# Performance work log

Measured on AMD Instinct MI355X. Metric: run time of the kernel, lower is better.

The kernel has to match this reference:

```python
import jax, jax.numpy as jnp
import numpy as np

N_NODES = 50000
N_EDGES = 800000
IN_DIM = 64
OUT_DIM = 64
HID = OUT_DIM // 2  # 32
N_LAYERS = 9  # layer_num; layer_num >= 7 => no temporal conv, conv dropout unused


def _layernorm(x, w, b, eps=1e-5):
    mu = jnp.mean(x, axis=-1, keepdims=True)
    var = jnp.var(x, axis=-1, keepdims=True)
    return (x - mu) * jax.lax.rsqrt(var + eps) * w + b


def _conv(x, Wp, Wn, Ws, src, tgt, pos_m, neg_m):
    # relation-wise gather -> linear -> masked merge -> single scatter_add
    xs = x[src]  # [E, d_in]
    m = jnp.where(pos_m[:, None], xs @ Wp.T, 0.0) + jnp.where(neg_m[:, None], xs @ Wn.T, 0.0)
    agg = jax.ops.segment_sum(m, tgt, num_segments=N_NODES)
    return agg + x @ Ws.T


def _asfr(x, ln_w, ln_b, gw, gb):
    xn = _layernorm(x, ln_w, ln_b)
    w = jax.nn.sigmoid(xn @ gw.T + gb)
    w1 = jnp.where(w > 0.5, 1.0, w)
    w2 = jnp.where(w > 0.5, 0.0, w)
    x1 = w1 * x
    x2 = w2 * x
    h = x.shape[1] // 2
    return jnp.concatenate([x1[:, :h] + x2[:, h:], x1[:, h:] + x2[:, :h]], axis=1)


def setup_inputs() -> dict:
    key = jax.random.key(0)
    ks = jax.random.split(key, 24)
    init_emb = jax.random.normal(ks[0], (N_NODES, IN_DIM), dtype=jnp.float32)
    src = jax.random.randint(ks[1], (N_EDGES,), 0, N_NODES)
    tgt = jax.random.randint(ks[2], (N_EDGES,), 0, N_NODES)
    sign = jnp.where(jax.random.uniform(ks[3], (N_EDGES,)) > 0.5, 1, -1).astype(jnp.int64)
    edge_index_s = jnp.stack([src, tgt, sign], axis=1).astype(jnp.int64)

    def w(k, shape, fan_in):
        return jax.random.normal(k, shape, dtype=jnp.float32) * (1.0 / np.sqrt(fan_in))

    inp = dict(init_emb=init_emb, edge_index_s=edge_index_s)
    # conv1: in 64 -> 32, relations pos/neg + self loop (no bias)
    inp["W1_pos"] = w(ks[4], (HID, IN_DIM), IN_DIM)
    inp["W1_neg"] = w(ks[5], (HID, IN_DIM), IN_DIM)
    inp["W1_self"] = w(ks[6], (HID, IN_DIM), IN_DIM)
    # 8 further convs: 32 -> 32, stacked
    L = N_LAYERS - 1
    inp["Wl_pos"] = w(ks[7], (L, HID, HID), HID)
    inp["Wl_neg"] = w(ks[8], (L, HID, HID), HID)
    inp["Wl_self"] = w(ks[9], (L, HID, HID), HID)
    # ASFR
    inp["asfr_ln_w"] = jnp.ones((HID,), jnp.float32)
    inp["asfr_ln_b"] = jnp.zeros((HID,), jnp.float32)
    inp["asfr_gate_w"] = w(ks[10], (HID, HID), HID)
    inp["asfr_gate_b"] = jnp.zeros((HID,), jnp.float32)
    # projection 32 -> 64
    inp["proj_w"] = w(ks[11], (OUT_DIM, HID), HID)
    inp["proj_b"] = jnp.zeros((OUT_DIM,), jnp.float32)
    # readout MLP: 64 -> 64 -> 64 -> 1, layernorm + relu between
    inp["mlp_w1"] = w(ks[12], (OUT_DIM, OUT_DIM), OUT_DIM)
    inp["mlp_b1"] = jnp.zeros((OUT_DIM,), jnp.float32)
    inp["mlp_ln1_w"] = jnp.ones((OUT_DIM,), jnp.float32)
    inp["mlp_ln1_b"] = jnp.zeros((OUT_DIM,), jnp.float32)
    inp["mlp_w2"] = w(ks[13], (OUT_DIM, OUT_DIM), OUT_DIM)
    inp["mlp_b2"] = jnp.zeros((OUT_DIM,), jnp.float32)
    inp["mlp_ln2_w"] = jnp.ones((OUT_DIM,), jnp.float32)
    inp["mlp_ln2_b"] = jnp.zeros((OUT_DIM,), jnp.float32)
    inp["mlp_w3"] = w(ks[14], (1, OUT_DIM), OUT_DIM)
    inp["mlp_b3"] = jnp.zeros((1,), jnp.float32)
    return inp


def reference(init_emb, edge_index_s, W1_pos, W1_neg, W1_self, Wl_pos, Wl_neg, Wl_self,
              asfr_ln_w, asfr_ln_b, asfr_gate_w, asfr_gate_b, proj_w, proj_b,
              mlp_w1, mlp_b1, mlp_ln1_w, mlp_ln1_b, mlp_w2, mlp_b2,
              mlp_ln2_w, mlp_ln2_b, mlp_w3, mlp_b3):
    src = edge_index_s[:, 0]
    tgt = edge_index_s[:, 1]
    sign = edge_index_s[:, 2]
    pos_m = sign > 0
    neg_m = sign < 0

    z = jax.nn.elu(_conv(init_emb, W1_pos, W1_neg, W1_self, src, tgt, pos_m, neg_m))
    z = _asfr(z, asfr_ln_w, asfr_ln_b, asfr_gate_w, asfr_gate_b)
    for i in range(Wl_pos.shape[0]):
        z_new = jax.nn.elu(_conv(z, Wl_pos[i], Wl_neg[i], Wl_self[i], src, tgt, pos_m, neg_m))
        z = z_new if i == 0 else z_new + 0.1 * z
    z = jax.nn.elu(z @ proj_w.T + proj_b)
    # readout MLP (eval mode: dropout identity)
    h = jax.nn.relu(_layernorm(z @ mlp_w1.T + mlp_b1, mlp_ln1_w, mlp_ln1_b))
    h = jax.nn.relu(_layernorm(h @ mlp_w2.T + mlp_b2, mlp_ln2_w, mlp_ln2_b))
    prob = jax.nn.sigmoid(h @ mlp_w3.T + mlp_b3)
    return (z, prob)
```

## Files before the change

### kernel.cpp

```cpp
#include <hip/hip_runtime.h>
#include <hip/hip_bf16.h>

#define NODES 50000
#define EDGES 800000
#define BSH 8
#define NBUCK 196
#define NBIN_BLOCKS 391

__device__ __forceinline__ float elu1(float x) { return x > 0.f ? x : expm1f(x); }

union F4 { float4 v; float f[4]; };

__global__ __launch_bounds__(256) void k_bhist(const int* __restrict__ ei, int* __restrict__ bucket_cnt) {
  __shared__ int cnt[NBUCK];
  int t = threadIdx.x;
  for (int i = t; i < NBUCK; i += 256) cnt[i] = 0;
  __syncthreads();
  int base = blockIdx.x * 2048;
#pragma unroll
  for (int i = 0; i < 8; i++) {
    int e = base + i * 256 + t;
    if (e < EDGES) atomicAdd(&cnt[ei[e * 3 + 1] >> BSH], 1);
  }
  __syncthreads();
  for (int i = t; i < NBUCK; i += 256)
    if (cnt[i]) atomicAdd(bucket_cnt + i, cnt[i]);
}

__global__ __launch_bounds__(256) void k_bscan(const int* __restrict__ bucket_cnt,
                                               int* __restrict__ bucket_base,
                                               int* __restrict__ bucket_cursor) {
  __shared__ int s[256];
  int t = threadIdx.x;
  int v = (t < NBUCK) ? bucket_cnt[t] : 0;
  s[t] = v;
  __syncthreads();
  for (int o = 1; o < 256; o <<= 1) {
    int x = (t >= o) ? s[t - o] : 0;
    __syncthreads();
    s[t] += x;
    __syncthreads();
  }
  if (t < NBUCK) { int e = s[t] - v; bucket_base[t] = e; bucket_cursor[t] = e; }
}

__global__ __launch_bounds__(256) void k_bin(const int* __restrict__ ei,
                                             int* __restrict__ bucket_cursor,
                                             unsigned* __restrict__ binned) {
  __shared__ int cnt[NBUCK], basec[NBUCK];
  int t = threadIdx.x;
  for (int i = t; i < NBUCK; i += 256) cnt[i] = 0;
  __syncthreads();
  int eb = blockIdx.x * 2048;
#pragma unroll
  for (int i = 0; i < 8; i++) {
    int e = eb + i * 256 + t;
    if (e < EDGES) atomicAdd(&cnt[ei[e * 3 + 1] >> BSH], 1);
  }
  __syncthreads();
  for (int i = t; i < NBUCK; i += 256) {
    int c = cnt[i];
    basec[i] = c ? atomicAdd(bucket_cursor + i, c) : 0;
    cnt[i] = 0;
  }
  __syncthreads();
#pragma unroll
  for (int i = 0; i < 8; i++) {
    int e = eb + i * 256 + t;
    if (e < EDGES) {
      int src = ei[e * 3 + 0];
      int tgt = ei[e * 3 + 1];
      int sg  = ei[e * 3 + 2];
      unsigned val = (unsigned)src | (sg < 0 ? 0x10000u : 0u) | ((unsigned)(tgt & 255) << 17);
      int bkt = tgt >> BSH;
      int r = atomicAdd(&cnt[bkt], 1);
      binned[basec[bkt] + r] = val;
    }
  }
}

__global__ __launch_bounds__(256) void k_scatter2(const unsigned* __restrict__ binned,
                                                  const int* __restrict__ bucket_base,
                                                  const int* __restrict__ bucket_cnt,
                                                  int* __restrict__ offs,
                                                  unsigned* __restrict__ perm) {
  __shared__ int cnt[256];
  __shared__ int s[256];
  int b = blockIdx.x, t = threadIdx.x;
  int t0 = b << BSH;
  cnt[t] = 0;
  __syncthreads();
  int n = bucket_cnt[b], bb = bucket_base[b];
  for (int i = t; i < n; i += 256) atomicAdd(&cnt[(binned[bb + i] >> 17) & 255], 1);
  __syncthreads();
  int v = cnt[t];
  s[t] = v;
  __syncthreads();
  for (int o = 1; o < 256; o <<= 1) {
    int x = (t >= o) ? s[t - o] : 0;
    __syncthreads();
    s[t] += x;
    __syncthreads();
  }
  int pos = bb + s[t] - v;
  if (t0 + t < NODES) offs[t0 + t] = pos;
  cnt[t] = pos;
  if (b == 0 && t == 0) offs[NODES] = EDGES;
  __syncthreads();
  for (int i = t; i < n; i += 256) {
    unsigned e = binned[bb + i];
    int p = atomicAdd(&cnt[(e >> 17) & 255], 1);
    perm[p] = (e & 0xFFFFu) | ((e & 0x10000u) << 15);
  }
}

__global__ __launch_bounds__(256) void k_lin64(const float* __restrict__ x,
    const float* __restrict__ Wp, const float* __restrict__ Wn, const float* __restrict__ Ws,
    __hip_bfloat16* __restrict__ ypb, __hip_bfloat16* __restrict__ ynb,
    unsigned short* __restrict__ ysb) {
  constexpr int K4 = 16;
  __shared__ float4 wp[K4][32], wn[K4][32], wsm[K4][32];
  __shared__ float4 xs[8][K4];
  for (int i = threadIdx.x; i < 32 * K4; i += 256) {
    int k4 = i >> 5, c = i & 31;
    wp[k4][c]  = ((const float4*)Wp)[c * K4 + k4];
    wn[k4][c]  = ((const float4*)Wn)[c * K4 + k4];
    wsm[k4][c] = ((const float4*)Ws)[c * K4 + k4];
  }
  int base = blockIdx.x * 8;
  for (int i = threadIdx.x; i < 8 * K4; i += 256) {
    int r = i / K4, k4 = i - r * K4;
    xs[r][k4] = ((const float4*)(x + (size_t)(base + r) * 64))[k4];
  }
  __syncthreads();
  int lane = threadIdx.x & 31, local = threadIdx.x >> 5;
  float ap = 0.f, an = 0.f, asf = 0.f;
#pragma unroll
  for (int k4 = 0; k4 < K4; k4++) {
    float4 xv = xs[local][k4];
    float4 a = wp[k4][lane], b = wn[k4][lane], c = wsm[k4][lane];
    ap  = fmaf(xv.w, a.w, fmaf(xv.z, a.z, fmaf(xv.y, a.y, fmaf(xv.x, a.x, ap))));
    an  = fmaf(xv.w, b.w, fmaf(xv.z, b.z, fmaf(xv.y, b.y, fmaf(xv.x, b.x, an))));
    asf = fmaf(xv.w, c.w, fmaf(xv.z, c.z, fmaf(xv.y, c.y, fmaf(xv.x, c.x, asf))));
  }
  size_t o = (size_t)(base + local) * 32 + lane;
  ypb[o] = __float2bfloat16(ap);
  ynb[o] = __float2bfloat16(an);
  ysb[o] = __bfloat16_as_ushort(__float2bfloat16(asf));
}

#define ACC8(A, V)                                   \
  A[0] += __uint_as_float((V).x << 16);              \
  A[1] += __uint_as_float((V).x & 0xffff0000u);      \
  A[2] += __uint_as_float((V).y << 16);              \
  A[3] += __uint_as_float((V).y & 0xffff0000u);      \
  A[4] += __uint_as_float((V).z << 16);              \
  A[5] += __uint_as_float((V).z & 0xffff0000u);      \
  A[6] += __uint_as_float((V).w << 16);              \
  A[7] += __uint_as_float((V).w & 0xffff0000u);

template <int DO_ASFR, int DO_RES, int DO_LIN, int WRITE_Z>
__global__ __launch_bounds__(256) void k_layer(
    const unsigned short* __restrict__ ypi, const unsigned short* __restrict__ yni,
    unsigned short* __restrict__ ysb,
    const unsigned* __restrict__ perm, const int* __restrict__ offs,
    float* __restrict__ z,
    const float* __restrict__ lnw, const float* __restrict__ lnb,
    const float* __restrict__ gw, const float* __restrict__ gb,
    const float* __restrict__ Wp, const float* __restrict__ Wn, const float* __restrict__ Ws,
    __hip_bfloat16* __restrict__ ypo, __hip_bfloat16* __restrict__ yno) {
  __shared__ float4 wps[8][32], wns[8][32], wss[8][32], gws[8][32];
  __shared__ float zrow[8][36], xrow[8][36];
  int t = threadIdx.x;
  if (DO_LIN) {
    int k4 = t >> 5, c = t & 31;
    wps[k4][c] = ((const float4*)Wp)[c * 8 + k4];
    wns[k4][c] = ((const float4*)Wn)[c * 8 + k4];
    wss[k4][c] = ((const float4*)Ws)[c * 8 + k4];
    if (DO_ASFR) gws[k4][c] = ((const float4*)gw)[c * 8 + k4];
  }
  int lane = t & 31, local = t >> 5;
  int node = blockIdx.x * 8 + local;
  int es = lane >> 2, fs = lane & 3;
  int beg = offs[node], end = offs[node + 1];
  float a0[8], a1[8], a2[8], a3[8];
#pragma unroll
  for (int i = 0; i < 8; i++) { a0[i] = 0.f; a1[i] = 0.f; a2[i] = 0.f; a3[i] = 0.f; }
  for (int base = beg; base < end; base += 32) {
    unsigned pe = (base + lane < end) ? perm[base + lane] : 0u;
    int rem = end - base;
    unsigned u0 = __shfl(pe, es, 32);
    unsigned u1 = __shfl(pe, es + 8, 32);
    const unsigned short* p0 = (u0 >> 31) ? yni : ypi;
    const unsigned short* p1 = (u1 >> 31) ? yni : ypi;
    uint4 v0 = *((const uint4*)(p0 + (size_t)(u0 & 0x7FFFFFFFu) * 32) + fs);
    uint4 v1 = *((const uint4*)(p1 + (size_t)(u1 & 0x7FFFFFFFu) * 32) + fs);
    if (es < rem) { ACC8(a0, v0); }
    if (es + 8 < rem) { ACC8(a1, v1); }
    if (rem > 16) {
      unsigned u2 = __shfl(pe, es + 16, 32);
      unsigned u3 = __shfl(pe, es + 24, 32);
      const unsigned short* p2 = (u2 >> 31) ? yni : ypi;
      const unsigned short* p3 = (u3 >> 31) ? yni : ypi;
      uint4 v2 = *((const uint4*)(p2 + (size_t)(u2 & 0x7FFFFFFFu) * 32) + fs);
      uint4 v3 = *((const uint4*)(p3 + (size_t)(u3 & 0x7FFFFFFFu) * 32) + fs);
      if (es + 16 < rem) { ACC8(a2, v2); }
      if (es + 24 < rem) { ACC8(a3, v3); }
    }
  }
#pragma unroll
  for (int i = 0; i < 8; i++) a0[i] += (a1[i] + a2[i]) + a3[i];
#pragma unroll
  for (int m = 4; m <= 16; m <<= 1) {
#pragma unroll
    for (int i = 0; i < 8; i++) a0[i] += __shfl_xor(a0[i], m, 32);
  }
  if (es == 0) {
    uint4 sv = *((const uint4*)(ysb + (size_t)node * 32) + fs);
    float sf[8];
    sf[0] = __uint_as_float(sv.x << 16); sf[1] = __uint_as_float(sv.x & 0xffff0000u);
    sf[2] = __uint_as_float(sv.y << 16); sf[3] = __uint_as_float(sv.y & 0xffff0000u);
    sf[4] = __uint_as_float(sv.z << 16); sf[5] = __uint_as_float(sv.z & 0xffff0000u);
    sf[6] = __uint_as_float(sv.w << 16); sf[7] = __uint_as_float(sv.w & 0xffff0000u);
    float o[8];
#pragma unroll
    for (int i = 0; i < 8; i++) o[i] = elu1(a0[i] + sf[i]);
    if (DO_RES) {
      const float* rr = z + (size_t)node * 32 + fs * 8;
      F4 r0, r1;
      r0.v = *(const float4*)rr;
      r1.v = *(const float4*)(rr + 4);
#pragma unroll
      for (int i = 0; i < 4; i++) { o[i] += 0.1f * r0.f[i]; o[4 + i] += 0.1f * r1.f[i]; }
    }
#pragma unroll
    for (int i = 0; i < 8; i++) zrow[local][fs * 8 + i] = o[i];
    if (WRITE_Z) {
      float* zw = z + (size_t)node * 32 + fs * 8;
      *(float4*)zw = make_float4(o[0], o[1], o[2], o[3]);
      *(float4*)(zw + 4) = make_float4(o[4], o[5], o[6], o[7]);
    }
  }
  __syncthreads();
  if (!DO_LIN) return;
  if (DO_ASFR) {
    float v = zrow[local][lane];
    float s = v;
#pragma unroll
    for (int m = 16; m; m >>= 1) s += __shfl_xor(s, m, 32);
    float mu = s * (1.f / 32.f);
    float d = v - mu, sq = d * d;
#pragma unroll
    for (int m = 16; m; m >>= 1) sq += __shfl_xor(sq, m, 32);
    float xn = d * rsqrtf(sq * (1.f / 32.f) + 1e-5f) * lnw[lane] + lnb[lane];
    xrow[local][lane] = xn;
    float ga = gb[lane];
#pragma unroll
    for (int k4 = 0; k4 < 8; k4++) {
      float4 xv = *((const float4*)&xrow[local][0] + k4);
      float4 w = gws[k4][lane];
      ga = fmaf(xv.w, w.w, fmaf(xv.z, w.z, fmaf(xv.y, w.y, fmaf(xv.x, w.x, ga))));
    }
    float g = 1.f / (1.f + __expf(-ga));
    float w1 = g > 0.5f ? 1.f : g;
    float w2 = g > 0.5f ? 0.f : g;
    float zn = w1 * v + __shfl_xor(w2 * v, 16, 32);
    zrow[local][lane] = zn;
  }
  float ap = 0.f, an = 0.f, asf = 0.f;
#pragma unroll
  for (int k4 = 0; k4 < 8; k4++) {
    float4 xv = *((const float4*)&zrow[local][0] + k4);
    float4 a2w = wps[k4][lane], b2 = wns[k4][lane], c2 = wss[k4][lane];
    ap  = fmaf(xv.w, a2w.w, fmaf(xv.z, a2w.z, fmaf(xv.y, a2w.y, fmaf(xv.x, a2w.x, ap))));
    an  = fmaf(xv.w, b2.w, fmaf(xv.z, b2.z, fmaf(xv.y, b2.y, fmaf(xv.x, b2.x, an))));
    asf = fmaf(xv.w, c2.w, fmaf(xv.z, c2.z, fmaf(xv.y, c2.y, fmaf(xv.x, c2.x, asf))));
  }
  size_t o = (size_t)node * 32 + lane;
  ypo[o] = __float2bfloat16(ap);
  yno[o] = __float2bfloat16(an);
  ysb[o] = __bfloat16_as_ushort(__float2bfloat16(asf));
}

__global__ __launch_bounds__(256) void k_mlp(const float* __restrict__ z,
    const float* __restrict__ pw, const float* __restrict__ pb,
    const float* __restrict__ w1, const float* __restrict__ b1,
    const float* __restrict__ l1w, const float* __restrict__ l1b,
    const float* __restrict__ w2, const float* __restrict__ b2,
    const float* __restrict__ l2w, const float* __restrict__ l2b,
    const float* __restrict__ w3, const float* __restrict__ b3,
    float* __restrict__ outz, float* __restrict__ outp) {
  __shared__ float4 wbuf[1536];
  __shared__ float4 hbuf4[128 * 17];
  __shared__ float pb_s[64], b1_s[64], l1w_s[64], l1b_s[64], b2_s[64], l2w_s[64], l2b_s[64], w3_s[64];
  int t = threadIdx.x;
  for (int i = t; i < 512; i += 256) {
    int k = i >> 4, j4 = i & 15;
    float4 v;
    v.x = pw[(j4 * 4 + 0) * 32 + k]; v.y = pw[(j4 * 4 + 1) * 32 + k];
    v.z = pw[(j4 * 4 + 2) * 32 + k]; v.w = pw[(j4 * 4 + 3) * 32 + k];
    wbuf[i] = v;
  }
  for (int i = t; i < 1024; i += 256) {
    int k = i >> 4, j4 = i & 15;
    float4 v;
    v.x = w1[(j4 * 4 + 0) * 64 + k]; v.y = w1[(j4 * 4 + 1) * 64 + k];
    v.z = w1[(j4 * 4 + 2) * 64 + k]; v.w = w1[(j4 * 4 + 3) * 64 + k];
    wbuf[512 + i] = v;
  }
  if (t < 64) {
    pb_s[t] = pb[t]; b1_s[t] = b1[t]; l1w_s[t] = l1w[t]; l1b_s[t] = l1b[t];
    b2_s[t] = b2[t]; l2w_s[t] = l2w[t]; l2b_s[t] = l2b[t]; w3_s[t] = w3[t];
  }
  __syncthreads();
  int g = t >> 3, q = t & 7;
  int nb0 = blockIdx.x * 128 + g;
  float bb3 = b3[0];
  bool live[4];
#pragma unroll
  for (int n = 0; n < 4; n++) live[n] = (nb0 + 32 * n) < NODES;
  float acc[4][8], h[4][8];
#pragma unroll
  for (int n = 0; n < 4; n++)
    if (live[n])
      hbuf4[(n * 32 + g) * 17 + q] = ((const float4*)(z + (size_t)(nb0 + 32 * n) * 32))[q];
#pragma unroll
  for (int n = 0; n < 4; n++)
#pragma unroll
    for (int i = 0; i < 8; i++) acc[n][i] = pb_s[q * 8 + i];
#pragma unroll 2
  for (int k4 = 0; k4 < 8; k4++) {
    F4 hv[4];
#pragma unroll
    for (int n = 0; n < 4; n++) hv[n].v = hbuf4[(n * 32 + g) * 17 + k4];
#pragma unroll
    for (int c = 0; c < 4; c++) {
      float4 wa = wbuf[(k4 * 4 + c) * 16 + q * 2];
      float4 wb = wbuf[(k4 * 4 + c) * 16 + q * 2 + 1];
#pragma unroll
      for (int n = 0; n < 4; n++) {
        float hk = hv[n].f[c];
        acc[n][0] = fmaf(hk, wa.x, acc[n][0]); acc[n][1] = fmaf(hk, wa.y, acc[n][1]);
        acc[n][2] = fmaf(hk, wa.z, acc[n][2]); acc[n][3] = fmaf(hk, wa.w, acc[n][3]);
        acc[n][4] = fmaf(hk, wb.x, acc[n][4]); acc[n][5] = fmaf(hk, wb.y, acc[n][5]);
        acc[n][6] = fmaf(hk, wb.z, acc[n][6]); acc[n][7] = fmaf(hk, wb.w, acc[n][7]);
      }
    }
  }
#pragma unroll
  for (int n = 0; n < 4; n++) {
#pragma unroll
    for (int i = 0; i < 8; i++) h[n][i] = elu1(acc[n][i]);
    float4 h0 = make_float4(h[n][0], h[n][1], h[n][2], h[n][3]);
    float4 h1 = make_float4(h[n][4], h[n][5], h[n][6], h[n][7]);
    if (live[n]) {
      float4* oz = (float4*)(outz + (size_t)(nb0 + 32 * n) * 64 + q * 8);
      oz[0] = h0; oz[1] = h1;
    }
    hbuf4[(n * 32 + g) * 17 + 2 * q] = h0;
    hbuf4[(n * 32 + g) * 17 + 2 * q + 1] = h1;
  }
#pragma unroll
  for (int n = 0; n < 4; n++)
#pragma unroll
    for (int i = 0; i < 8; i++) acc[n][i] = b1_s[q * 8 + i];
#pragma unroll 2
  for (int k4 = 0; k4 < 16; k4++) {
    F4 hv[4];
#pragma unroll
    for (int n = 0; n < 4; n++) hv[n].v = hbuf4[(n * 32 + g) * 17 + k4];
#pragma unroll
    for (int c = 0; c < 4; c++) {
      float4 wa = wbuf[512 + (k4 * 4 + c) * 16 + q * 2];
      float4 wb = wbuf[512 + (k4 * 4 + c) * 16 + q * 2 + 1];
#pragma unroll
      for (int n = 0; n < 4; n++) {
        float hk = hv[n].f[c];
        acc[n][0] = fmaf(hk, wa.x, acc[n][0]); acc[n][1] = fmaf(hk, wa.y, acc[n][1]);
        acc[n][2] = fmaf(hk, wa.z, acc[n][2]); acc[n][3] = fmaf(hk, wa.w, acc[n][3]);
        acc[n][4] = fmaf(hk, wb.x, acc[n][4]); acc[n][5] = fmaf(hk, wb.y, acc[n][5]);
        acc[n][6] = fmaf(hk, wb.z, acc[n][6]); acc[n][7] = fmaf(hk, wb.w, acc[n][7]);
      }
    }
  }
  __syncthreads();
  for (int i = t; i < 1024; i += 256) {
    int k = i >> 4, j4 = i & 15;
    float4 v;
    v.x = w2[(j4 * 4 + 0) * 64 + k]; v.y = w2[(j4 * 4 + 1) * 64 + k];
    v.z = w2[(j4 * 4 + 2) * 64 + k]; v.w = w2[(j4 * 4 + 3) * 64 + k];
    wbuf[i] = v;
  }
#pragma unroll
  for (int n = 0; n < 4; n++) {
    float s = 0.f;
#pragma unroll
    for (int i = 0; i < 8; i++) s += acc[n][i];
    s += __shfl_xor(s, 1, 8); s += __shfl_xor(s, 2, 8); s += __shfl_xor(s, 4, 8);
    float mu = s * (1.f / 64.f);
    float vs = 0.f;
#pragma unroll
    for (int i = 0; i < 8; i++) { float dd = acc[n][i] - mu; vs += dd * dd; }
    vs += __shfl_xor(vs, 1, 8); vs += __shfl_xor(vs, 2, 8); vs += __shfl_xor(vs, 4, 8);
    float rs = rsqrtf(vs * (1.f / 64.f) + 1e-5f);
#pragma unroll
    for (int i = 0; i < 8; i++)
      h[n][i] = fmaxf((acc[n][i] - mu) * rs * l1w_s[q * 8 + i] + l1b_s[q * 8 + i], 0.f);
  }
  __syncthreads();
#pragma unroll
  for (int n = 0; n < 4; n++) {
    hbuf4[(n * 32 + g) * 17 + 2 * q] = make_float4(h[n][0], h[n][1], h[n][2], h[n][3]);
    hbuf4[(n * 32 + g) * 17 + 2 * q + 1] = make_float4(h[n][4], h[n][5], h[n][6], h[n][7]);
  }
#pragma unroll
  for (int n = 0; n < 4; n++)
#pragma unroll
    for (int i = 0; i < 8; i++) acc[n][i] = b2_s[q * 8 + i];
#pragma unroll 2
  for (int k4 = 0; k4 < 16; k4++) {
    F4 hv[4];
#pragma unroll
    for (int n = 0; n < 4; n++) hv[n].v = hbuf4[(n * 32 + g) * 17 + k4];
#pragma unroll
    for (int c = 0; c < 4; c++) {
      float4 wa = wbuf[(k4 * 4 + c) * 16 + q * 2];
      float4 wb = wbuf[(k4 * 4 + c) * 16 + q * 2 + 1];
#pragma unroll
      for (int n = 0; n < 4; n++) {
        float hk = hv[n].f[c];
        acc[n][0] = fmaf(hk, wa.x, acc[n][0]); acc[n][1] = fmaf(hk, wa.y, acc[n][1]);
        acc[n][2] = fmaf(hk, wa.z, acc[n][2]); acc[n][3] = fmaf(hk, wa.w, acc[n][3]);
        acc[n][4] = fmaf(hk, wb.x, acc[n][4]); acc[n][5] = fmaf(hk, wb.y, acc[n][5]);
        acc[n][6] = fmaf(hk, wb.z, acc[n][6]); acc[n][7] = fmaf(hk, wb.w, acc[n][7]);
      }
    }
  }
#pragma unroll
  for (int n = 0; n < 4; n++) {
    float s = 0.f;
#pragma unroll
    for (int i = 0; i < 8; i++) s += acc[n][i];
    s += __shfl_xor(s, 1, 8); s += __shfl_xor(s, 2, 8); s += __shfl_xor(s, 4, 8);
    float mu = s * (1.f / 64.f);
    float vs = 0.f;
#pragma unroll
    for (int i = 0; i < 8; i++) { float dd = acc[n][i] - mu; vs += dd * dd; }
    vs += __shfl_xor(vs, 1, 8); vs += __shfl_xor(vs, 2, 8); vs += __shfl_xor(vs, 4, 8);
    float rs = rsqrtf(vs * (1.f / 64.f) + 1e-5f);
    float p = 0.f;
#pragma unroll
    for (int i = 0; i < 8; i++) {
      float hv2 = fmaxf((acc[n][i] - mu) * rs * l2w_s[q * 8 + i] + l2b_s[q * 8 + i], 0.f);
      p = fmaf(hv2, w3_s[q * 8 + i], p);
    }
    p += __shfl_xor(p, 1, 8); p += __shfl_xor(p, 2, 8); p += __shfl_xor(p, 4, 8);
    if (q == 0 && live[n]) outp[nb0 + 32 * n] = 1.f / (1.f + __expf(-(p + bb3)));
  }
}

extern "C" void kernel_launch(void* const* d_in, const int* in_sizes, int n_in,
                              void* d_out, int out_size, void* d_ws, size_t ws_size,
                              hipStream_t stream) {
  const float* init_emb = (const float*)d_in[0];
  const int*   ei  = (const int*)d_in[1];
  const float* W1p = (const float*)d_in[2];
  const float* W1n = (const float*)d_in[3];
  const float* W1s = (const float*)d_in[4];
  const float* Wlp = (const float*)d_in[5];
  const float* Wln = (const float*)d_in[6];
  const float* Wls = (const float*)d_in[7];
  const float* lnw = (const float*)d_in[8];
  const float* lnb = (const float*)d_in[9];
  const float* gw  = (const float*)d_in[10];
  const float* gb  = (const float*)d_in[11];
  const float* pw  = (const float*)d_in[12];
  const float* pb  = (const float*)d_in[13];
  const float* w1  = (const float*)d_in[14];
  const float* b1  = (const float*)d_in[15];
  const float* l1w = (const float*)d_in[16];
  const float* l1b = (const float*)d_in[17];
  const float* w2  = (const float*)d_in[18];
  const float* b2  = (const float*)d_in[19];
  const float* l2w = (const float*)d_in[20];
  const float* l2b = (const float*)d_in[21];
  const float* w3  = (const float*)d_in[22];
  const float* b3  = (const float*)d_in[23];

  char* ws = (char*)d_ws;
  size_t off = 0;
  auto alloc = [&](size_t b) { void* p = ws + off; off = (off + b + 255) & ~(size_t)255; return p; };
  __hip_bfloat16* ypA = (__hip_bfloat16*)alloc(NODES * 32 * 2);
  __hip_bfloat16* ynA = (__hip_bfloat16*)alloc(NODES * 32 * 2);
  __hip_bfloat16* ypB = (__hip_bfloat16*)alloc(NODES * 32 * 2);
  __hip_bfloat16* ynB = (__hip_bfloat16*)alloc(NODES * 32 * 2);
  unsigned short* ysb = (unsigned short*)alloc(NODES * 32 * 2);
  float*    zbuf   = (float*)alloc(NODES * 32 * 4);
  unsigned* perm   = (unsigned*)alloc(EDGES * 4);
  int*      offs   = (int*)alloc((NODES + 1) * 4);
  int*      bucket_cnt    = (int*)alloc(NBUCK * 4);
  int*      bucket_base   = (int*)alloc(NBUCK * 4);
  int*      bucket_cursor = (int*)alloc(NBUCK * 4);
  unsigned* binned = (unsigned*)ypA;

  hipMemsetAsync(bucket_cnt, 0, NBUCK * 4, stream);
  k_bhist<<<NBIN_BLOCKS, 256, 0, stream>>>(ei, bucket_cnt);
  k_bscan<<<1, 256, 0, stream>>>(bucket_cnt, bucket_base, bucket_cursor);
  k_bin<<<NBIN_BLOCKS, 256, 0, stream>>>(ei, bucket_cursor, binned);
  k_scatter2<<<NBUCK, 256, 0, stream>>>(binned, bucket_base, bucket_cnt, offs, perm);

  const int G = NODES / 8;
  k_lin64<<<G, 256, 0, stream>>>(init_emb, W1p, W1n, W1s, ypA, ynA, ysb);
  k_layer<1, 0, 1, 0><<<G, 256, 0, stream>>>((const unsigned short*)ypA, (const unsigned short*)ynA,
      ysb, perm, offs, zbuf, lnw, lnb, gw, gb, Wlp, Wln, Wls, ypB, ynB);
  k_layer<0, 0, 1, 1><<<G, 256, 0, stream>>>((const unsigned short*)ypB, (const unsigned short*)ynB,
      ysb, perm, offs, zbuf, nullptr, nullptr, nullptr, nullptr,
      Wlp + 1024, Wln + 1024, Wls + 1024, ypA, ynA);
  const __hip_bfloat16* yin_p = ypA; const __hip_bfloat16* yin_n = ynA;
  __hip_bfloat16* yout_p = ypB; __hip_bfloat16* yout_n = ynB;
  for (int i = 1; i < 7; i++) {
    k_layer<0, 1, 1, 1><<<G, 256, 0, stream>>>((const unsigned short*)yin_p, (const unsigned short*)yin_n,
        ysb, perm, offs, zbuf, nullptr, nullptr, nullptr, nullptr,
        Wlp + (i + 1) * 1024, Wln + (i + 1) * 1024, Wls + (i + 1) * 1024, yout_p, yout_n);
    const __hip_bfloat16* tp = yin_p; const __hip_bfloat16* tn = yin_n;
    yin_p = yout_p; yin_n = yout_n;
    yout_p = (__hip_bfloat16*)tp; yout_n = (__hip_bfloat16*)tn;
  }
  k_layer<0, 1, 0, 1><<<G, 256, 0, stream>>>((const unsigned short*)yin_p, (const unsigned short*)yin_n,
      ysb, perm, offs, zbuf, nullptr, nullptr, nullptr, nullptr,
      nullptr, nullptr, nullptr, nullptr, nullptr);

  float* outz = (float*)d_out;
  float* outp = outz + (size_t)NODES * 64;
  k_mlp<<<(NODES + 127) / 128, 256, 0, stream>>>(zbuf, pw, pb, w1, b1, l1w, l1b,
                                                 w2, b2, l2w, l2b, w3, b3, outz, outp);
}
```

Baseline: 345.9 us.

## Interleave pos/neg bf16 features, precompute byte offsets, and loop 4 node groups per block

Stores the positive and negative projected features interleaved in a single [N,64] bf16 buffer and encodes each edge in perm as a direct byte offset, so the gather drops the pointer select and the multiply. Each layer block now handles 4 groups of 8 nodes, which amortises the shared-memory weight load and cuts the grid size. The sync is only taken on the first iteration, so zrow/xrow reuse across later groups depends on each warp touching only its own row. Packing the byte offset into 32 bits limits the node count to about 2^25.

```diff
diff --git a/kernel.cpp b/kernel.cpp
--- a/kernel.cpp
+++ b/kernel.cpp
@@ -6,6 +6,9 @@
 #define BSH 8
 #define NBUCK 196
 #define NBIN_BLOCKS 391
+#define NGRP 6250
+#define GPB 4
+#define LGRID 1563
 
 __device__ __forceinline__ float elu1(float x) { return x > 0.f ? x : expm1f(x); }
 
@@ -110,14 +113,13 @@
   for (int i = t; i < n; i += 256) {
     unsigned e = binned[bb + i];
     int p = atomicAdd(&cnt[(e >> 17) & 255], 1);
-    perm[p] = (e & 0xFFFFu) | ((e & 0x10000u) << 15);
+    perm[p] = ((e & 0xFFFFu) << 7) | ((e & 0x10000u) >> 10);
   }
 }
 
 __global__ __launch_bounds__(256) void k_lin64(const float* __restrict__ x,
     const float* __restrict__ Wp, const float* __restrict__ Wn, const float* __restrict__ Ws,
-    __hip_bfloat16* __restrict__ ypb, __hip_bfloat16* __restrict__ ynb,
-    unsigned short* __restrict__ ysb) {
+    unsigned short* __restrict__ ypn, unsigned short* __restrict__ ysb) {
   constexpr int K4 = 16;
   __shared__ float4 wp[K4][32], wn[K4][32], wsm[K4][32];
   __shared__ float4 xs[8][K4];
@@ -143,10 +145,11 @@
     an  = fmaf(xv.w, b.w, fmaf(xv.z, b.z, fmaf(xv.y, b.y, fmaf(xv.x, b.x, an))));
     asf = fmaf(xv.w, c.w, fmaf(xv.z, c.z, fmaf(xv.y, c.y, fmaf(xv.x, c.x, asf))));
   }
-  size_t o = (size_t)(base + local) * 32 + lane;
-  ypb[o] = __float2bfloat16(ap);
-  ynb[o] = __float2bfloat16(an);
-  ysb[o] = __bfloat16_as_ushort(__float2bfloat16(asf));
+  int node = base + local;
+  size_t o64 = (size_t)node * 64 + lane;
+  ypn[o64]      = __bfloat16_as_ushort(__float2bfloat16(ap));
+  ypn[o64 + 32] = __bfloat16_as_ushort(__float2bfloat16(an));
+  ysb[(size_t)node * 32 + lane] = __bfloat16_as_ushort(__float2bfloat16(asf));
 }
 
 #define ACC8(A, V)                                   \
@@ -161,14 +164,14 @@
 
 template <int DO_ASFR, int DO_RES, int DO_LIN, int WRITE_Z>
 __global__ __launch_bounds__(256) void k_layer(
-    const unsigned short* __restrict__ ypi, const unsigned short* __restrict__ yni,
+    const unsigned short* __restrict__ ypni,
     unsigned short* __restrict__ ysb,
     const unsigned* __restrict__ perm, const int* __restrict__ offs,
     float* __restrict__ z,
     const float* __restrict__ lnw, const float* __restrict__ lnb,
     const float* __restrict__ gw, const float* __restrict__ gb,
     const float* __restrict__ Wp, const float* __restrict__ Wn, const float* __restrict__ Ws,
-    __hip_bfloat16* __restrict__ ypo, __hip_bfloat16* __restrict__ yno) {
+    unsigned short* __restrict__ ypno) {
   __shared__ float4 wps[8][32], wns[8][32], wss[8][32], gws[8][32];
   __shared__ float zrow[8][36], xrow[8][36];
   int t = threadIdx.x;
@@ -180,106 +183,107 @@
     if (DO_ASFR) gws[k4][c] = ((const float4*)gw)[c * 8 + k4];
   }
   int lane = t & 31, local = t >> 5;
-  int node = blockIdx.x * 8 + local;
   int es = lane >> 2, fs = lane & 3;
-  int beg = offs[node], end = offs[node + 1];
-  float a0[8], a1[8], a2[8], a3[8];
-#pragma unroll
-  for (int i = 0; i < 8; i++) { a0[i] = 0.f; a1[i] = 0.f; a2[i] = 0.f; a3[i] = 0.f; }
-  for (int base = beg; base < end; base += 32) {
-    unsigned pe = (base + lane < end) ? perm[base + lane] : 0u;
-    int rem = end - base;
-    unsigned u0 = __shfl(pe, es, 32);
-    unsigned u1 = __shfl(pe, es + 8, 32);
-    const unsigned short* p0 = (u0 >> 31) ? yni : ypi;
-    const unsigned short* p1 = (u1 >> 31) ? yni : ypi;
-    uint4 v0 = *((const uint4*)(p0 + (size_t)(u0 & 0x7FFFFFFFu) * 32) + fs);
-    uint4 v1 = *((const uint4*)(p1 + (size_t)(u1 & 0x7FFFFFFFu) * 32) + fs);
-    if (es < rem) { ACC8(a0, v0); }
-    if (es + 8 < rem) { ACC8(a1, v1); }
-    if (rem > 16) {
-      unsigned u2 = __shfl(pe, es + 16, 32);
-      unsigned u3 = __shfl(pe, es + 24, 32);
-      const unsigned short* p2 = (u2 >> 31) ? yni : ypi;
-      const unsigned short* p3 = (u3 >> 31) ? yni : ypi;
-      uint4 v2 = *((const uint4*)(p2 + (size_t)(u2 & 0x7FFFFFFFu) * 32) + fs);
-      uint4 v3 = *((const uint4*)(p3 + (size_t)(u3 & 0x7FFFFFFFu) * 32) + fs);
-      if (es + 16 < rem) { ACC8(a2, v2); }
-      if (es + 24 < rem) { ACC8(a3, v3); }
-    }
-  }
-#pragma unroll
-  for (int i = 0; i < 8; i++) a0[i] += (a1[i] + a2[i]) + a3[i];
-#pragma unroll
-  for (int m = 4; m <= 16; m <<= 1) {
-#pragma unroll
-    for (int i = 0; i < 8; i++) a0[i] += __shfl_xor(a0[i], m, 32);
-  }
-  if (es == 0) {
-    uint4 sv = *((const uint4*)(ysb + (size_t)node * 32) + fs);
-    float sf[8];
-    sf[0] = __uint_as_float(sv.x << 16); sf[1] = __uint_as_float(sv.x & 0xffff0000u);
-    sf[2] = __uint_as_float(sv.y << 16); sf[3] = __uint_as_float(sv.y & 0xffff0000u);
-    sf[4] = __uint_as_float(sv.z << 16); sf[5] = __uint_as_float(sv.z & 0xffff0000u);
-    sf[6] = __uint_as_float(sv.w << 16); sf[7] = __uint_as_float(sv.w & 0xffff0000u);
-    float o[8];
-#pragma unroll
-    for (int i = 0; i < 8; i++) o[i] = elu1(a0[i] + sf[i]);
-    if (DO_RES) {
-      const float* rr = z + (size_t)node * 32 + fs * 8;
-      F4 r0, r1;
-      r0.v = *(const float4*)rr;
-      r1.v = *(const float4*)(rr + 4);
-#pragma unroll
-      for (int i = 0; i < 4; i++) { o[i] += 0.1f * r0.f[i]; o[4 + i] += 0.1f * r1.f[i]; }
-    }
-#pragma unroll
-    for (int i = 0; i < 8; i++) zrow[local][fs * 8 + i] = o[i];
-    if (WRITE_Z) {
-      float* zw = z + (size_t)node * 32 + fs * 8;
-      *(float4*)zw = make_float4(o[0], o[1], o[2], o[3]);
-      *(float4*)(zw + 4) = make_float4(o[4], o[5], o[6], o[7]);
-    }
-  }
-  __syncthreads();
-  if (!DO_LIN) return;
-  if (DO_ASFR) {
-    float v = zrow[local][lane];
-    float s = v;
-#pragma unroll
-    for (int m = 16; m; m >>= 1) s += __shfl_xor(s, m, 32);
-    float mu = s * (1.f / 32.f);
-    float d = v - mu, sq = d * d;
-#pragma unroll
-    for (int m = 16; m; m >>= 1) sq += __shfl_xor(sq, m, 32);
-    float xn = d * rsqrtf(sq * (1.f / 32.f) + 1e-5f) * lnw[lane] + lnb[lane];
-    xrow[local][lane] = xn;
-    float ga = gb[lane];
+  const char* ybase = (const char*)ypni;
+  int g0 = blockIdx.x * GPB;
+  int gend = (g0 + GPB < NGRP) ? g0 + GPB : NGRP;
+  for (int gi = g0; gi < gend; gi++) {
+    int node = gi * 8 + local;
+    int beg = offs[node], end = offs[node + 1];
+    float a0[8], a1[8], a2[8], a3[8];
+#pragma unroll
+    for (int i = 0; i < 8; i++) { a0[i] = 0.f; a1[i] = 0.f; a2[i] = 0.f; a3[i] = 0.f; }
+    for (int base = beg; base < end; base += 32) {
+      unsigned pe = (base + lane < end) ? perm[base + lane] : 0u;
+      int rem = end - base;
+      unsigned u0 = __shfl(pe, es, 32);
+      unsigned u1 = __shfl(pe, es + 8, 32);
+      uint4 v0 = *(const uint4*)(ybase + u0 + fs * 16);
+      uint4 v1 = *(const uint4*)(ybase + u1 + fs * 16);
+      if (es < rem) { ACC8(a0, v0); }
+      if (es + 8 < rem) { ACC8(a1, v1); }
+      if (rem > 16) {
+        unsigned u2 = __shfl(pe, es + 16, 32);
+        unsigned u3 = __shfl(pe, es + 24, 32);
+        uint4 v2 = *(const uint4*)(ybase + u2 + fs * 16);
+        uint4 v3 = *(const uint4*)(ybase + u3 + fs * 16);
+        if (es + 16 < rem) { ACC8(a2, v2); }
+        if (es + 24 < rem) { ACC8(a3, v3); }
+      }
+    }
+#pragma unroll
+    for (int i = 0; i < 8; i++) a0[i] += (a1[i] + a2[i]) + a3[i];
+#pragma unroll
+    for (int m = 4; m <= 16; m <<= 1) {
+#pragma unroll
+      for (int i = 0; i < 8; i++) a0[i] += __shfl_xor(a0[i], m, 32);
+    }
+    if (es == 0) {
+      uint4 sv = *((const uint4*)(ysb + (size_t)node * 32) + fs);
+      float sf[8];
+      sf[0] = __uint_as_float(sv.x << 16); sf[1] = __uint_as_float(sv.x & 0xffff0000u);
+      sf[2] = __uint_as_float(sv.y << 16); sf[3] = __uint_as_float(sv.y & 0xffff0000u);
+      sf[4] = __uint_as_float(sv.z << 16); sf[5] = __uint_as_float(sv.z & 0xffff0000u);
+      sf[6] = __uint_as_float(sv.w << 16); sf[7] = __uint_as_float(sv.w & 0xffff0000u);
+      float o[8];
+#pragma unroll
+      for (int i = 0; i < 8; i++) o[i] = elu1(a0[i] + sf[i]);
+      if (DO_RES) {
+        const float* rr = z + (size_t)node * 32 + fs * 8;
+        F4 r0, r1;
+        r0.v = *(const float4*)rr;
+        r1.v = *(const float4*)(rr + 4);
+#pragma unroll
+        for (int i = 0; i < 4; i++) { o[i] += 0.1f * r0.f[i]; o[4 + i] += 0.1f * r1.f[i]; }
+      }
+#pragma unroll
+      for (int i = 0; i < 8; i++) zrow[local][fs * 8 + i] = o[i];
+      if (WRITE_Z) {
+        float* zw = z + (size_t)node * 32 + fs * 8;
+        *(float4*)zw = make_float4(o[0], o[1], o[2], o[3]);
+        *(float4*)(zw + 4) = make_float4(o[4], o[5], o[6], o[7]);
+      }
+    }
+    if (gi == g0 && DO_LIN) __syncthreads();
+    if (!DO_LIN) continue;
+    if (DO_ASFR) {
+      float v = zrow[local][lane];
+      float s = v;
+#pragma unroll
+      for (int m = 16; m; m >>= 1) s += __shfl_xor(s, m, 32);
+      float mu = s * (1.f / 32.f);
+      float d = v - mu, sq = d * d;
+#pragma unroll
+      for (int m = 16; m; m >>= 1) sq += __shfl_xor(sq, m, 32);
+      float xn = d * rsqrtf(sq * (1.f / 32.f) + 1e-5f) * lnw[lane] + lnb[lane];
+      xrow[local][lane] = xn;
+      float ga = gb[lane];
+#pragma unroll
+      for (int k4 = 0; k4 < 8; k4++) {
+        float4 xv = *((const float4*)&xrow[local][0] + k4);
+        float4 w = gws[k4][lane];
+        ga = fmaf(xv.w, w.w, fmaf(xv.z, w.z, fmaf(xv.y, w.y, fmaf(xv.x, w.x, ga))));
+      }
+      float g = 1.f / (1.f + __expf(-ga));
+      float w1 = g > 0.5f ? 1.f : g;
+      float w2 = g > 0.5f ? 0.f : g;
+      float zn = w1 * v + __shfl_xor(w2 * v, 16, 32);
+      zrow[local][lane] = zn;
+    }
+    float ap = 0.f, an = 0.f, asf = 0.f;
 #pragma unroll
     for (int k4 = 0; k4 < 8; k4++) {
-      float4 xv = *((const float4*)&xrow[local][0] + k4);
-      float4 w = gws[k4][lane];
-      ga = fmaf(xv.w, w.w, fmaf(xv.z, w.z, fmaf(xv.y, w.y, fmaf(xv.x, w.x, ga))));
-    }
-    float g = 1.f / (1.f + __expf(-ga));
-    float w1 = g > 0.5f ? 1.f : g;
-    float w2 = g > 0.5f ? 0.f : g;
-    float zn = w1 * v + __shfl_xor(w2 * v, 16, 32);
-    zrow[local][lane] = zn;
-  }
-  float ap = 0.f, an = 0.f, asf = 0.f;
-#pragma unroll
-  for (int k4 = 0; k4 < 8; k4++) {
-    float4 xv = *((const float4*)&zrow[local][0] + k4);
-    float4 a2w = wps[k4][lane], b2 = wns[k4][lane], c2 = wss[k4][lane];
-    ap  = fmaf(xv.w, a2w.w, fmaf(xv.z, a2w.z, fmaf(xv.y, a2w.y, fmaf(xv.x, a2w.x, ap))));
-    an  = fmaf(xv.w, b2.w, fmaf(xv.z, b2.z, fmaf(xv.y, b2.y, fmaf(xv.x, b2.x, an))));
-    asf = fmaf(xv.w, c2.w, fmaf(xv.z, c2.z, fmaf(xv.y, c2.y, fmaf(xv.x, c2.x, asf))));
-  }
-  size_t o = (size_t)node * 32 + lane;
-  ypo[o] = __float2bfloat16(ap);
-  yno[o] = __float2bfloat16(an);
-  ysb[o] = __bfloat16_as_ushort(__float2bfloat16(asf));
+      float4 xv = *((const float4*)&zrow[local][0] + k4);
+      float4 a2w = wps[k4][lane], b2 = wns[k4][lane], c2 = wss[k4][lane];
+      ap  = fmaf(xv.w, a2w.w, fmaf(xv.z, a2w.z, fmaf(xv.y, a2w.y, fmaf(xv.x, a2w.x, ap))));
+      an  = fmaf(xv.w, b2.w, fmaf(xv.z, b2.z, fmaf(xv.y, b2.y, fmaf(xv.x, b2.x, an))));
+      asf = fmaf(xv.w, c2.w, fmaf(xv.z, c2.z, fmaf(xv.y, c2.y, fmaf(xv.x, c2.x, asf))));
+    }
+    size_t o64 = (size_t)node * 64 + lane;
+    ypno[o64]      = __bfloat16_as_ushort(__float2bfloat16(ap));
+    ypno[o64 + 32] = __bfloat16_as_ushort(__float2bfloat16(an));
+    ysb[(size_t)node * 32 + lane] = __bfloat16_as_ushort(__float2bfloat16(asf));
+  }
 }
 
 __global__ __launch_bounds__(256) void k_mlp(const float* __restrict__ z,
@@ -490,18 +494,16 @@
   char* ws = (char*)d_ws;
   size_t off = 0;
   auto alloc = [&](size_t b) { void* p = ws + off; off = (off + b + 255) & ~(size_t)255; return p; };
-  __hip_bfloat16* ypA = (__hip_bfloat16*)alloc(NODES * 32 * 2);
-  __hip_bfloat16* ynA = (__hip_bfloat16*)alloc(NODES * 32 * 2);
-  __hip_bfloat16* ypB = (__hip_bfloat16*)alloc(NODES * 32 * 2);
-  __hip_bfloat16* ynB = (__hip_bfloat16*)alloc(NODES * 32 * 2);
-  unsigned short* ysb = (unsigned short*)alloc(NODES * 32 * 2);
-  float*    zbuf   = (float*)alloc(NODES * 32 * 4);
-  unsigned* perm   = (unsigned*)alloc(EDGES * 4);
+  unsigned short* ypnA = (unsigned short*)alloc((size_t)NODES * 64 * 2);
+  unsigned short* ypnB = (unsigned short*)alloc((size_t)NODES * 64 * 2);
+  unsigned short* ysb  = (unsigned short*)alloc((size_t)NODES * 32 * 2);
+  float*    zbuf   = (float*)alloc((size_t)NODES * 32 * 4);
+  unsigned* perm   = (unsigned*)alloc((size_t)EDGES * 4);
   int*      offs   = (int*)alloc((NODES + 1) * 4);
   int*      bucket_cnt    = (int*)alloc(NBUCK * 4);
   int*      bucket_base   = (int*)alloc(NBUCK * 4);
   int*      bucket_cursor = (int*)alloc(NBUCK * 4);
-  unsigned* binned = (unsigned*)ypA;
+  unsigned* binned = (unsigned*)ypnA;
 
   hipMemsetAsync(bucket_cnt, 0, NBUCK * 4, stream);
   k_bhist<<<NBIN_BLOCKS, 256, 0, stream>>>(ei, bucket_cnt);
@@ -509,26 +511,22 @@
   k_bin<<<NBIN_BLOCKS, 256, 0, stream>>>(ei, bucket_cursor, binned);
   k_scatter2<<<NBUCK, 256, 0, stream>>>(binned, bucket_base, bucket_cnt, offs, perm);
 
-  const int G = NODES / 8;
-  k_lin64<<<G, 256, 0, stream>>>(init_emb, W1p, W1n, W1s, ypA, ynA, ysb);
-  k_layer<1, 0, 1, 0><<<G, 256, 0, stream>>>((const unsigned short*)ypA, (const unsigned short*)ynA,
-      ysb, perm, offs, zbuf, lnw, lnb, gw, gb, Wlp, Wln, Wls, ypB, ynB);
-  k_layer<0, 0, 1, 1><<<G, 256, 0, stream>>>((const unsigned short*)ypB, (const unsigned short*)ynB,
-      ysb, perm, offs, zbuf, nullptr, nullptr, nullptr, nullptr,
-      Wlp + 1024, Wln + 1024, Wls + 1024, ypA, ynA);
-  const __hip_bfloat16* yin_p = ypA; const __hip_bfloat16* yin_n = ynA;
-  __hip_bfloat16* yout_p = ypB; __hip_bfloat16* yout_n = ynB;
+  k_lin64<<<NODES / 8, 256, 0, stream>>>(init_emb, W1p, W1n, W1s, ypnA, ysb);
+
+  k_layer<1, 0, 1, 0><<<LGRID, 256, 0, stream>>>(ypnA, ysb, perm, offs, zbuf,
+      lnw, lnb, gw, gb, Wlp, Wln, Wls, ypnB);
+  k_layer<0, 0, 1, 1><<<LGRID, 256, 0, stream>>>(ypnB, ysb, perm, offs, zbuf,
+      nullptr, nullptr, nullptr, nullptr, Wlp + 1024, Wln + 1024, Wls + 1024, ypnA);
+  unsigned short* yin = ypnA;
+  unsigned short* yout = ypnB;
   for (int i = 1; i < 7; i++) {
-    k_layer<0, 1, 1, 1><<<G, 256, 0, stream>>>((const unsigned short*)yin_p, (const unsigned short*)yin_n,
-        ysb, perm, offs, zbuf, nullptr, nullptr, nullptr, nullptr,
-        Wlp + (i + 1) * 1024, Wln + (i + 1) * 1024, Wls + (i + 1) * 1024, yout_p, yout_n);
-    const __hip_bfloat16* tp = yin_p; const __hip_bfloat16* tn = yin_n;
-    yin_p = yout_p; yin_n = yout_n;
-    yout_p = (__hip_bfloat16*)tp; yout_n = (__hip_bfloat16*)tn;
-  }
-  k_layer<0, 1, 0, 1><<<G, 256, 0, stream>>>((const unsigned short*)yin_p, (const unsigned short*)yin_n,
-      ysb, perm, offs, zbuf, nullptr, nullptr, nullptr, nullptr,
-      nullptr, nullptr, nullptr, nullptr, nullptr);
+    k_layer<0, 1, 1, 1><<<LGRID, 256, 0, stream>>>(yin, ysb, perm, offs, zbuf,
+        nullptr, nullptr, nullptr, nullptr,
+        Wlp + (i + 1) * 1024, Wln + (i + 1) * 1024, Wls + (i + 1) * 1024, yout);
+    unsigned short* tp = yin; yin = yout; yout = tp;
+  }
+  k_layer<0, 1, 0, 1><<<LGRID, 256, 0, stream>>>(yin, ysb, perm, offs, zbuf,
+      nullptr, nullptr, nullptr, nullptr, nullptr, nullptr, nullptr, nullptr);
 
   float* outz = (float*)d_out;
   float* outp = outz + (size_t)NODES * 64;
```

After: 404.2 us. +16.9%, slower.
